# Optimization experiments

Measured on AMD Instinct MI355X. Metric: run time of the kernel, lower is better.

## Reference

```python
import math
import jax, jax.numpy as jnp
import numpy as np
from jax.scipy.special import erf

D = 128                # cubic box / image size (even)
B, T = 4, 2            # particles, candidate poses per particle
GRID_DIST_DEGS = 8.0
GRID_STEP_DEGS = 2.0
PIXEL_SIZE = 1.5       # Angstrom / px
MAX_SHIFT_FRACTION = 0.2
TOP_K = 2
HALF_PARTICLE = 0.5 * D


def _rot_z(a):
    c, s = jnp.cos(a), jnp.sin(a)
    z, o = jnp.zeros_like(a), jnp.ones_like(a)
    return jnp.stack([jnp.stack([c, -s, z], -1),
                      jnp.stack([s, c, z], -1),
                      jnp.stack([z, z, o], -1)], -2)


def _rot_y(a):
    c, s = jnp.cos(a), jnp.sin(a)
    z, o = jnp.zeros_like(a), jnp.ones_like(a)
    return jnp.stack([jnp.stack([c, z, s], -1),
                      jnp.stack([z, o, z], -1),
                      jnp.stack([-s, z, c], -1)], -2)


def _euler_zyz_to_matrix(ang):
    # RELION convention ZYZ: R = Rz(a) @ Ry(b) @ Rz(c)
    return _rot_z(ang[..., 0]) @ _rot_y(ang[..., 1]) @ _rot_z(ang[..., 2])


def _so3_grid_rotmats():
    n = math.ceil(GRID_DIST_DEGS / GRID_STEP_DEGS)
    n = n if n % 2 == 1 else n + 1
    half = GRID_DIST_DEGS / 2.0
    a = np.linspace(-half, half, n)
    g = np.stack(np.meshgrid(a, a, a, indexing='ij'), -1).reshape(-1, 3)
    return _euler_zyz_to_matrix(jnp.deg2rad(jnp.asarray(g, jnp.float32)))


def _compute_dft(vol):
    # sinc^2 gridding pre-filter, then fftshifted rfftn of fftshifted volume
    d = vol.shape[-1]
    f = jnp.fft.fftshift(jnp.fft.fftfreq(d)).astype(vol.dtype)
    fz, fy, fx = jnp.meshgrid(f, f, f, indexing='ij')
    r = jnp.sqrt(fz * fz + fy * fy + fx * fx)
    vol = vol * jnp.sinc(r) ** 2
    dft = jnp.fft.rfftn(jnp.fft.fftshift(vol, axes=(-3, -2, -1)), axes=(-3, -2, -1))
    return jnp.fft.fftshift(dft, axes=(-3, -2))


def _trilinear_complex(vol, z, y, x):
    # trilinear interpolation into a complex 3D array, zero outside bounds
    Dz, Dy, Dx = vol.shape
    z0f, y0f, x0f = jnp.floor(z), jnp.floor(y), jnp.floor(x)
    fz, fy, fx = z - z0f, y - y0f, x - x0f
    z0, y0, x0 = z0f.astype(jnp.int32), y0f.astype(jnp.int32), x0f.astype(jnp.int32)

    def corner(zi, yi, xi, w):
        valid = (zi >= 0) & (zi < Dz) & (yi >= 0) & (yi < Dy) & (xi >= 0) & (xi < Dx)
        v = vol[jnp.clip(zi, 0, Dz - 1), jnp.clip(yi, 0, Dy - 1), jnp.clip(xi, 0, Dx - 1)]
        return jnp.where(valid, v * w, jnp.zeros((), vol.dtype))

    out = corner(z0, y0, x0, (1 - fz) * (1 - fy) * (1 - fx))
    out = out + corner(z0, y0, x0 + 1, (1 - fz) * (1 - fy) * fx)
    out = out + corner(z0, y0 + 1, x0, (1 - fz) * fy * (1 - fx))
    out = out + corner(z0, y0 + 1, x0 + 1, (1 - fz) * fy * fx)
    out = out + corner(z0 + 1, y0, x0, fz * (1 - fy) * (1 - fx))
    out = out + corner(z0 + 1, y0, x0 + 1, fz * (1 - fy) * fx)
    out = out + corner(z0 + 1, y0 + 1, x0, fz * fy * (1 - fx))
    out = out + corner(z0 + 1, y0 + 1, x0 + 1, fz * fy * fx)
    return out


def _extract_central_slices_rfft_3d(vol_rfft, d, rotmats):
    # rotated central-slice extraction from a fftshifted rfft 3D volume
    fy = jnp.fft.fftshift(jnp.fft.fftfreq(d)).astype(jnp.float32)
    fx = jnp.fft.rfftfreq(d).astype(jnp.float32)
    gy, gx = jnp.meshgrid(fy, fx, indexing='ij')            # (H, Wr)
    coords = jnp.stack([jnp.zeros_like(gy), gy, gx], -1)    # zyx, z=0 plane
    Rzyx = rotmats[..., ::-1, ::-1]                         # xyz rotmat -> zyx
    rot = jnp.einsum('...ij,hwj->...hwi', Rzyx, coords)     # (...,H,Wr,3)
    conj_mask = rot[..., 2] < 0                             # redundant half
    rot = jnp.where(conj_mask[..., None], -rot, rot)
    zi = rot[..., 0] * d + d // 2
    yi = rot[..., 1] * d + d // 2
    xi = rot[..., 2] * d
    s = _trilinear_complex(vol_rfft, zi, yi, xi)
    return jnp.where(conj_mask, jnp.conj(s), s)


def _forward(vol, imgs, ctf, rotmats, grid_rotmats):
    d = vol.shape[-1]
    vol_rfft = _compute_dft(vol)                            # (d, d, d//2+1)
    # _real_to_fourier
    fimg = jnp.fft.fftshift(
        jnp.fft.rfftn(jnp.fft.fftshift(imgs, axes=(-2, -1)), axes=(-2, -1)),
        axes=(-2,))                                         # (B, d, d//2+1)
    # compose pose candidates with the local SO3 grid: rotmats @ grid_rotmats
    exp_R = jnp.einsum('gjk,btij->btgik', grid_rotmats, rotmats)   # (B,T,G,3,3)
    projs = _extract_central_slices_rfft_3d(vol_rfft, d, exp_R)    # (B,T,G,H,Wr)
    projs = projs * ctf[:, None, None]
    # correlate_dft_2d
    prod = fimg[:, None, None] * jnp.conj(projs)
    prod = jnp.fft.ifftshift(prod, axes=(-2,))
    corrs = jnp.fft.ifftshift(jnp.fft.irfftn(prod, s=(d, d), axes=(-2, -1)),
                              axes=(-2, -1))                # (B,T,G,d,d) real
    # constrained peak search within max_shift_fraction window
    delta = math.ceil(d * (1.0 - MAX_SHIFT_FRACTION) / 2)
    h0 = delta
    c = corrs[..., h0:d - delta, h0:d - delta]
    maxJ = jnp.max(c, -1)
    argJ = jnp.argmax(c, -1)
    perImgCorr = jnp.max(maxJ, -1)                          # (B,T,G)
    argI = jnp.argmax(maxJ, -1)
    col = jnp.take_along_axis(argJ, argI[..., None], -1)[..., 0]
    shiftsXY = jnp.stack([h0 + col, h0 + argI], -1)         # (B,T,G,2) as (x,y)
    b = perImgCorr.shape[0]
    nrots = perImgCorr.shape[2]
    flat = perImgCorr.reshape(b, -1)                        # (B, T*G)
    maxCorrs, maxIdxs = jax.lax.top_k(flat, TOP_K)
    bestShifts = jnp.take_along_axis(shiftsXY.reshape(b, -1, 2),
                                     maxIdxs[..., None], axis=1)   # (B,K,2)
    mean = jnp.mean(flat, -1, keepdims=True)
    std = jnp.std(flat, -1, keepdims=True, ddof=1)
    comparedWeight = 0.5 * (1.0 + erf((maxCorrs - mean) / (std * 1.4142135623730951)))
    predShiftsAngs = -(bestShifts.astype(jnp.float32) - HALF_PARTICLE) * PIXEL_SIZE
    predRotMats = grid_rotmats[maxIdxs % nrots]             # (B,K,3,3)
    return maxCorrs, predRotMats, predShiftsAngs, comparedWeight


def setup_inputs() -> dict:
    key = jax.random.key(0)
    kv, ki, kc, kr = jax.random.split(key, 4)
    vol = jax.random.normal(kv, (D, D, D), jnp.float32)
    imgs = jax.random.normal(ki, (B, D, D), jnp.float32)
    ctf = jax.random.uniform(kc, (B, D, D // 2 + 1), jnp.float32, -1.0, 1.0)
    ang = jax.random.uniform(kr, (B, T, 3), jnp.float32, -np.pi, np.pi)
    rotmats = _euler_zyz_to_matrix(ang)
    grid_rotmats = _so3_grid_rotmats()
    return {"vol": vol, "imgs": imgs, "ctf": ctf, "rotmats": rotmats,
            "grid_rotmats": grid_rotmats}


def reference(vol, imgs, ctf, rotmats, grid_rotmats):
    return _forward(vol, imgs, ctf, rotmats, grid_rotmats)
```

## Files before the change

### kernel.cpp

```cpp
#include <hip/hip_runtime.h>
#include <math.h>
#include <float.h>

#define DD   128
#define KX   65
#define NB   4
#define NTT  2
#define NG   125
#define NBTG (NB*NTT*NG)
#define WIN  24
#define H0   52

#define PZ  132
#define PY  132
#define PX  68
#define PROW  PX
#define PPLANE (PY*PX)
#define HALO_N 119872

typedef float f4 __attribute__((ext_vector_type(4), aligned(8)));

__device__ __forceinline__ float2 cmul(float2 a, float2 b){
    return make_float2(a.x*b.x - a.y*b.y, a.x*b.y + a.y*b.x);
}

__device__ __forceinline__ void make_tw(float2* sTw, int tid){
    if (tid < 128){
        float s, c;
        sincosf((float)tid * (float)(M_PI/64.0), &s, &c);
        sTw[tid] = make_float2(c, s);
    }
}

__global__ __launch_bounds__(256) void k_stageA(const float* __restrict__ vol,
                       const float* __restrict__ imgs,
                       float2* __restrict__ A1, float2* __restrict__ B1){
    __shared__ float2 sZ [16*DD];
    __shared__ float2 sZ2[16*DD];
    __shared__ float2 sTw[128];
    int tid = threadIdx.x;
    int bid = blockIdx.x;
    make_tw(sTw, tid);
    __syncthreads();

    if (bid < 512){
        int z = bid >> 2, q = bid & 3;
        int y0 = q*32;
        float fz = (z-64)*(1.0f/128.0f);
        for (int i = tid; i < 16*DD; i += 256){
            int p = i >> 7, x = i & 127;
            int yA = y0 + 2*p;
            float fx = (x-64)*(1.0f/128.0f);
            float fyA = (yA-64)*(1.0f/128.0f);
            float fyB = fyA + (1.0f/128.0f);
            float b2 = fz*fz + fx*fx;
            float rA = sqrtf(b2 + fyA*fyA);
            float rB = sqrtf(b2 + fyB*fyB);
            float sA = (rA > 0.f) ? (sinf((float)M_PI*rA)/((float)M_PI*rA)) : 1.f;
            float sB = (rB > 0.f) ? (sinf((float)M_PI*rB)/((float)M_PI*rB)) : 1.f;
            float a = vol[(z*DD + yA)*DD + x] * sA * sA;
            float b = vol[(z*DD + yA+1)*DD + x] * sB * sB;
            sZ[i] = make_float2(a, b);
        }
        __syncthreads();
        for (int i = tid; i < 16*32; i += 256){
            int p = i >> 5, x1 = i & 31;
            int b0 = p*DD + x1;
            float2 a = sZ[b0], bb = sZ[b0+32], c2 = sZ[b0+64], d = sZ[b0+96];
            float acx=a.x+c2.x, acy=a.y+c2.y;
            float amx=a.x-c2.x, amy=a.y-c2.y;
            float bdx=bb.x+d.x, bdy=bb.y+d.y;
            float bmx=bb.x-d.x, bmy=bb.y-d.y;
            sZ[b0   ] = make_float2(acx+bdx, acy+bdy);
            sZ[b0+32] = make_float2(amx+bmy, amy-bmx);
            sZ[b0+64] = make_float2(acx-bdx, acy-bdy);
            sZ[b0+96] = make_float2(amx-bmy, amy+bmx);
        }
        __syncthreads();
        for (int i = tid; i < 16*32; i += 256){
            int p = i >> 5, r5 = i & 31;
            int c = r5 >> 3, x2 = r5 & 7;
            int b0 = p*DD + 32*c + x2;
            float2 u0 = sZ[b0], u1 = sZ[b0+8], u2 = sZ[b0+16], u3 = sZ[b0+24];
            float2 w1 = sTw[(8*c)&127];  w1.y = -w1.y;
            float2 w2 = sTw[(16*c)&127]; w2.y = -w2.y;
            float2 w3 = sTw[(24*c)&127]; w3.y = -w3.y;
            float2 t1 = cmul(u1,w1), t2 = cmul(u2,w2), t3 = cmul(u3,w3);
            float2 pp = make_float2(u0.x+t2.x, u0.y+t2.y);
            float2 qq = make_float2(u0.x-t2.x, u0.y-t2.y);
            float2 rr = make_float2(t1.x+t3.x, t1.y+t3.y);
            float2 ss = make_float2(t1.x-t3.x, t1.y-t3.y);
            sZ[b0   ] = make_float2(pp.x+rr.x, pp.y+rr.y);
            sZ[b0+8 ] = make_float2(qq.x+ss.y, qq.y-ss.x);
            sZ[b0+16] = make_float2(pp.x-rr.x, pp.y-rr.y);
            sZ[b0+24] = make_float2(qq.x-ss.y, qq.y+ss.x);
        }
        __syncthreads();
        for (int i = tid; i < 16*DD; i += 256){
            int p = i >> 7, k = i & 127;
            int c = k & 3, s = (k >> 2) & 3;
            const float2* v = &sZ[p*DD + 32*c + 8*s];
            float ar0=0,ai0=0,ar1=0,ai1=0;
            int j = 0;
            #pragma unroll
            for (int x2 = 0; x2 < 8; x2 += 2){
                float2 v0 = v[x2], v1 = v[x2+1];
                float2 e0 = sTw[j]; int jn = (j + k)&127;
                float2 e1 = sTw[jn];
                ar0 += v0.x*e0.x + v0.y*e0.y;  ai0 += v0.y*e0.x - v0.x*e0.y;
                ar1 += v1.x*e1.x + v1.y*e1.y;  ai1 += v1.y*e1.x - v1.x*e1.y;
                j = (jn + k)&127;
            }
            sZ2[i] = make_float2(ar0+ar1, ai0+ai1);
        }
        __syncthreads();
        for (int i = tid; i < 16*KX; i += 256){
            int p = i / KX, k = i - p*KX;
            float2 Zk = sZ2[p*DD + k];
            float2 Zm = sZ2[p*DD + ((128-k)&127)];
            float2 A = make_float2(0.5f*(Zk.x+Zm.x), 0.5f*(Zk.y-Zm.y));
            float Dx = Zk.x - Zm.x, Dy = Zk.y + Zm.y;
            float2 Bv = make_float2(0.5f*Dy, -0.5f*Dx);
            int yA = y0 + 2*p;
            A1[(z*DD + yA  )*KX + k] = A;
            A1[(z*DD + yA+1)*KX + k] = Bv;
        }
    } else {
        int o = (bid - 512)*256 + tid;
        if (o >= NB*DD*KX) return;
        int b = o / (DD*KX);
        int r = o - b*DD*KX;
        int y = r / KX, k = r - y*KX;
        const float* row = imgs + (b*DD + y)*DD;
        float ar0=0,ai0=0,ar1=0,ai1=0,ar2=0,ai2=0,ar3=0,ai3=0;
        int i0=0, i1=k&127, i2=(2*k)&127, i3=(3*k)&127;
        int st = (4*k)&127;
        for (int x = 0; x < DD; x += 4){
            float v0=row[x], v1=row[x+1], v2=row[x+2], v3=row[x+3];
            float2 e0=sTw[i0], e1=sTw[i1], e2=sTw[i2], e3=sTw[i3];
            ar0 += v0*e0.x; ai0 -= v0*e0.y;
            ar1 += v1*e1.x; ai1 -= v1*e1.y;
            ar2 += v2*e2.x; ai2 -= v2*e2.y;
            ar3 += v3*e3.x; ai3 -= v3*e3.y;
            i0=(i0+st)&127; i1=(i1+st)&127; i2=(i2+st)&127; i3=(i3+st)&127;
        }
        B1[o] = make_float2(ar0+ar1+ar2+ar3, ai0+ai1+ai2+ai3);
    }
}

__global__ __launch_bounds__(256) void k_stageB(const float2* __restrict__ A1,
                       const float* __restrict__ ctf, const float2* __restrict__ B1,
                       float2* __restrict__ A2, float2* __restrict__ Fc){
    __shared__ float2 sU[32*KX];
    __shared__ float2 sTw[128];
    int tid = threadIdx.x;
    int bid = blockIdx.x;
    make_tw(sTw, tid);
    __syncthreads();

    if (bid < 512){
        int z = bid >> 2, c = bid & 3;
        const float2* base = A1 + z*DD*KX;
        for (int i = tid; i < 32*KX; i += 256){
            int n = i / KX, kk = i - n*KX;
            float2 a  = base[(n    )*KX + kk];
            float2 bb = base[(n+32)*KX + kk];
            float2 c2 = base[(n+64)*KX + kk];
            float2 d  = base[(n+96)*KX + kk];
            float acx = a.x + c2.x, acy = a.y + c2.y;
            float amx = a.x - c2.x, amy = a.y - c2.y;
            float bdx = bb.x + d.x, bdy = bb.y + d.y;
            float bmx = bb.x - d.x, bmy = bb.y - d.y;
            float2 u;
            if (c == 0)      u = make_float2(acx + bdx, acy + bdy);
            else if (c == 2) u = make_float2(acx - bdx, acy - bdy);
            else if (c == 1) u = make_float2(amx + bmy, amy - bmx);
            else             u = make_float2(amx - bmy, amy + bmx);
            sU[i] = u;
        }
        __syncthreads();
        float2 w1 = sTw[(8*c)&127];  w1.y = -w1.y;
        float2 w2 = sTw[(16*c)&127]; w2.y = -w2.y;
        float2 w3 = sTw[(24*c)&127]; w3.y = -w3.y;
        for (int i = tid; i < 8*KX; i += 256){
            int n2 = i / KX, kk = i - n2*KX;
            int b0 = n2*KX + kk;
            float2 u0 = sU[b0], u1 = sU[b0+8*KX], u2 = sU[b0+16*KX], u3 = sU[b0+24*KX];
            float2 t1 = cmul(u1,w1), t2 = cmul(u2,w2), t3 = cmul(u3,w3);
            float2 p = make_float2(u0.x+t2.x, u0.y+t2.y);
            float2 q = make_float2(u0.x-t2.x, u0.y-t2.y);
            float2 r = make_float2(t1.x+t3.x, t1.y+t3.y);
            float2 s = make_float2(t1.x-t3.x, t1.y-t3.y);
            sU[b0       ] = make_float2(p.x+r.x, p.y+r.y);
            sU[b0+ 8*KX ] = make_float2(q.x+s.y, q.y-s.x);
            sU[b0+16*KX ] = make_float2(p.x-r.x, p.y-r.y);
            sU[b0+24*KX ] = make_float2(q.x-s.y, q.y+s.x);
        }
        __syncthreads();
        for (int o = tid; o < 32*KX; o += 256){
            int m = o / KX, kk = o - m*KX;
            int ky = 4*m + c;
            int s4 = m & 3;
            const float2* v = &sU[(8*s4)*KX + kk];
            float ar0=0,ai0=0,ar1=0,ai1=0;
            int j = 0;
            #pragma unroll
            for (int n2 = 0; n2 < 8; n2 += 2){
                float2 v0 = v[n2*KX], v1 = v[(n2+1)*KX];
                float2 e0 = sTw[j]; int jn = (j + ky)&127;
                float2 e1 = sTw[jn];
                ar0 += v0.x*e0.x + v0.y*e0.y;  ai0 += v0.y*e0.x - v0.x*e0.y;
                ar1 += v1.x*e1.x + v1.y*e1.y;  ai1 += v1.y*e1.x - v1.x*e1.y;
                j = (jn + ky)&127;
            }
            A2[(z*DD + ky)*KX + kk] = make_float2(ar0+ar1, ai0+ai1);
        }
    } else {
        int o = (bid - 512)*256 + tid;
        if (o >= NB*DD*KX) return;
        int b = o / (DD*KX);
        int r = o - b*DD*KX;
        int h = r / KX, k = r - h*KX;
        int kky = (h + 64) & 127;
        const float2* col = B1 + b*DD*KX + k;
        float ar0=0,ai0=0,ar1=0,ai1=0,ar2=0,ai2=0,ar3=0,ai3=0;
        int i0=0, i1=kky&127, i2=(2*kky)&127, i3=(3*kky)&127;
        int st = (4*kky)&127;
        for (int y = 0; y < DD; y += 4){
            float2 v0=col[(y+0)*KX], v1=col[(y+1)*KX];
            float2 v2=col[(y+2)*KX], v3=col[(y+3)*KX];
            float2 e0=sTw[i0], e1=sTw[i1], e2=sTw[i2], e3=sTw[i3];
            ar0 += v0.x*e0.x + v0.y*e0.y;  ai0 += v0.y*e0.x - v0.x*e0.y;
            ar1 += v1.x*e1.x + v1.y*e1.y;  ai1 += v1.y*e1.x - v1.x*e1.y;
            ar2 += v2.x*e2.x + v2.y*e2.y;  ai2 += v2.y*e2.x - v2.x*e2.y;
            ar3 += v3.x*e3.x + v3.y*e3.y;  ai3 += v3.y*e3.x - v3.x*e3.y;
            i0=(i0+st)&127; i1=(i1+st)&127; i2=(i2+st)&127; i3=(i3+st)&127;
        }
        float sgn = ((h + k)&1) ? -1.f : 1.f;
        float cf = ctf[o];
        Fc[o] = make_float2((ar0+ar1+ar2+ar3)*sgn*cf, (ai0+ai1+ai2+ai3)*sgn*cf);
    }
}

__global__ __launch_bounds__(256) void k_volD(const float2* __restrict__ A2,
                       float2* __restrict__ VrP){
    __shared__ float2 sU[32*KX];
    __shared__ float2 sTw[128];
    int tid = threadIdx.x;
    int bid = blockIdx.x;
    int ky = bid >> 2, c = bid & 3;
    make_tw(sTw, tid);

    {
        int hidx = bid*256 + tid;
        if (hidx < HALO_N){
            int z, y, x;
            if (hidx < 35904){
                int p = hidx / 8976;
                int r = hidx - p*8976;
                z = (p == 0) ? 0 : (128 + p);
                y = r / 68;
                x = r - 68*y;
            } else if (hidx < 70720){
                int h2 = hidx - 35904;
                int zz = h2 / 272;
                int r = h2 - zz*272;
                z = 1 + zz;
                int p = r / 68;
                y = (p == 0) ? 0 : (128 + p);
                x = r - 68*p;
            } else {
                int h3 = hidx - 70720;
                int zz = h3 / 384;
                int r = h3 - zz*384;
                z = 1 + zz;
                y = 1 + r/3;
                x = 65 + (r - 3*(r/3));
            }
            VrP[(z*PY + y)*PX + x] = make_float2(0.f, 0.f);
        }
    }
    __syncthreads();

    const float2* base = A2 + ky*KX;
    for (int i = tid; i < 32*KX; i += 256){
        int n = i / KX, kk = i - n*KX;
        float2 a  = base[(n    )*DD*KX + kk];
        float2 bb = base[(n+32)*DD*KX + kk];
        float2 c2 = base[(n+64)*DD*KX + kk];
        float2 d  = base[(n+96)*DD*KX + kk];
        float acx = a.x + c2.x, acy = a.y + c2.y;
        float amx = a.x - c2.x, amy = a.y - c2.y;
        float bdx = bb.x + d.x, bdy = bb.y + d.y;
        float bmx = bb.x - d.x, bmy = bb.y - d.y;
        float2 u;
        if (c == 0)      u = make_float2(acx + bdx, acy + bdy);
        else if (c == 2) u = make_float2(acx - bdx, acy - bdy);
        else if (c == 1) u = make_float2(amx + bmy, amy - bmx);
        else             u = make_float2(amx - bmy, amy + bmx);
        sU[i] = u;
    }
    __syncthreads();
    float2 w1 = sTw[(8*c)&127];  w1.y = -w1.y;
    float2 w2 = sTw[(16*c)&127]; w2.y = -w2.y;
    float2 w3 = sTw[(24*c)&127]; w3.y = -w3.y;
    for (int i = tid; i < 8*KX; i += 256){
        int n2 = i / KX, kk = i - n2*KX;
        int b0 = n2*KX + kk;
        float2 u0 = sU[b0], u1 = sU[b0+8*KX], u2 = sU[b0+16*KX], u3 = sU[b0+24*KX];
        float2 t1 = cmul(u1,w1), t2 = cmul(u2,w2), t3 = cmul(u3,w3);
        float2 p = make_float2(u0.x+t2.x, u0.y+t2.y);
        float2 q = make_float2(u0.x-t2.x, u0.y-t2.y);
        float2 r = make_float2(t1.x+t3.x, t1.y+t3.y);
        float2 s = make_float2(t1.x-t3.x, t1.y-t3.y);
        sU[b0       ] = make_float2(p.x+r.x, p.y+r.y);
        sU[b0+ 8*KX ] = make_float2(q.x+s.y, q.y-s.x);
        sU[b0+16*KX ] = make_float2(p.x-r.x, p.y-r.y);
        sU[b0+24*KX ] = make_float2(q.x-s.y, q.y+s.x);
    }
    __syncthreads();
    int hy = (ky + 64) & 127;
    for (int o = tid; o < 32*KX; o += 256){
        int m = o / KX, kk = o - m*KX;
        int kz = 4*m + c;
        int hz = (kz + 64) & 127;
        int s4 = m & 3;
        const float2* v = &sU[(8*s4)*KX + kk];
        float ar0=0,ai0=0,ar1=0,ai1=0;
        int j = 0;
        #pragma unroll
        for (int n2 = 0; n2 < 8; n2 += 2){
            float2 v0 = v[n2*KX], v1 = v[(n2+1)*KX];
            float2 e0 = sTw[j]; int jn = (j + kz)&127;
            float2 e1 = sTw[jn];
            ar0 += v0.x*e0.x + v0.y*e0.y;  ai0 += v0.y*e0.x - v0.x*e0.y;
            ar1 += v1.x*e1.x + v1.y*e1.y;  ai1 += v1.y*e1.x - v1.x*e1.y;
            j = (jn + kz)&127;
        }
        float sgn = ((hz + hy + kk) & 1) ? -1.f : 1.f;
        VrP[((hz+1)*PY + (hy+1))*PX + kk] = make_float2((ar0+ar1)*sgn, (ai0+ai1)*sgn);
    }
}

__device__ __forceinline__ float2 slice_point(const float2* __restrict__ VrP,
        float2 f, float xi, float zi, float yi){
    bool neg = xi < 0.f;
    if (neg){ xi = -xi; zi = 128.f - zi; yi = 128.f - yi; }
    xi = fminf(xi, 65.f);
    zi = fminf(fmaxf(zi, -1.f), 129.f);
    yi = fminf(fmaxf(yi, -1.f), 129.f);
    float zf = floorf(zi), yf = floorf(yi), xf = floorf(xi);
    float fz = zi - zf, fy = yi - yf, fx = xi - xf;
    int z0 = (int)zf, y0 = (int)yf, x0 = (int)xf;
    int basei = ((z0+1)*PY + (y0+1))*PX + x0;
    f4 v00 = *reinterpret_cast<const f4*>(VrP + basei);
    f4 v01 = *reinterpret_cast<const f4*>(VrP + basei + PROW);
    f4 v10 = *reinterpret_cast<const f4*>(VrP + basei + PPLANE);
    f4 v11 = *reinterpret_cast<const f4*>(VrP + basei + PPLANE + PROW);
    float gx = 1.f - fx;
    float r00 = v00.x*gx + v00.z*fx, i00 = v00.y*gx + v00.w*fx;
    float r01 = v01.x*gx + v01.z*fx, i01 = v01.y*gx + v01.w*fx;
    float r10 = v10.x*gx + v10.z*fx, i10 = v10.y*gx + v10.w*fx;
    float r11 = v11.x*gx + v11.z*fx, i11 = v11.y*gx + v11.w*fx;
    float gz = 1.f - fz, gy = 1.f - fy;
    float w00 = gz*gy, w01 = gz*fy, w10 = fz*gy, w11 = fz*fy;
    float sr = r00*w00 + r01*w01 + r10*w10 + r11*w11;
    float si = i00*w00 + i01*w01 + i10*w10 + i11*w11;
    if (neg) si = -si;
    return make_float2(f.x*sr + f.y*si, f.y*sr - f.x*si);
}

__global__ __launch_bounds__(256,5) void k_main(
    const float2* __restrict__ VrP, const float2* __restrict__ Fc,
    const float* __restrict__ rotm, const float* __restrict__ grid,
    float* __restrict__ resVal, int2* __restrict__ resShift)
{
    __shared__ float2 sP[DD*16];
    __shared__ float2 sT[WIN*KX];
    __shared__ float2 sTw[128];
    __shared__ float  sM[9];
    __shared__ float  swv[4];
    __shared__ int    swi[4];

    int tid = threadIdx.x;
    int nb  = blockIdx.x;
    int blk = (nb & 7)*125 + (nb >> 3);
    int b  = blk / (NTT*NG);
    int rr = blk - b*NTT*NG;
    int t  = rr / NG;
    int g  = rr - t*NG;

    make_tw(sTw, tid);
    if (tid < 9){
        int i = tid/3, k = tid - 3*i;
        const float* R  = rotm + (b*NTT + t)*9;
        const float* Gm = grid + g*9;
        sM[tid] = R[i*3+0]*Gm[0*3+k] + R[i*3+1]*Gm[1*3+k] + R[i*3+2]*Gm[2*3+k];
    }
    __syncthreads();

    float M00=sM[0], M01=sM[1], M10=sM[3], M11=sM[4], M20=sM[6], M21=sM[7];
    const float2* FcB = Fc + b*DD*KX;

    if (tid < 128){
        int h = tid;
        float hf = (float)(h - 64);
        float xi = M01*hf + M00*64.f;
        float zi = M21*hf + M20*64.f + 64.f;
        float yi = M11*hf + M10*64.f + 64.f;
        sP[h] = slice_point(VrP, FcB[h*KX + 64], xi, zi, yi);
    }
    __syncthreads();
    if (tid < 96){
        int a = tid >> 2, p = tid & 3;
        int ry = (116 + a) & 127;
        int idx = (32*p*ry) & 127;
        float ar = 0.f, ai = 0.f;
        const float2* v = &sP[32*p];
        #pragma unroll 8
        for (int h2 = 0; h2 < 32; ++h2){
            float2 e = sTw[idx];
            float2 pv = v[h2];
            ar += pv.x*e.x - pv.y*e.y;
            ai += pv.x*e.y + pv.y*e.x;
            idx = (idx + ry) & 127;
        }
        sP[256 + tid] = make_float2(ar, ai);
    }
    __syncthreads();
    if (tid < 24){
        float2 p0 = sP[256 + tid*4 + 0];
        float2 p1 = sP[256 + tid*4 + 1];
        float2 p2 = sP[256 + tid*4 + 2];
        float2 p3 = sP[256 + tid*4 + 3];
        float sg = (tid & 1) ? -(1.f/128.f) : (1.f/128.f);
        sT[tid*KX + 64] = make_float2((p0.x+p1.x+p2.x+p3.x)*sg,
                                      (p0.y+p1.y+p2.y+p3.y)*sg);
    }
    __syncthreads();

    const int kk = tid & 15;
    const int h0 = tid >> 4;
    const float hf0 = (float)(h0 - 64);
    const float dxi = 16.f*M01, dzi = 16.f*M21, dyi = 16.f*M11;

    for (int cc = 0; cc < 4; ++cc){
        int w = cc*16 + kk;
        float wf = (float)w;
        float xi0 = M01*hf0 + M00*wf;
        float zi0 = M21*hf0 + M20*wf + 64.f;
        float yi0 = M11*hf0 + M10*wf + 64.f;
        int fidx = h0*KX + w;

        #pragma unroll 2
        for (int j = 0; j < 8; ++j){
            sP[tid + 256*j] = slice_point(VrP, FcB[fidx], xi0, zi0, yi0);
            xi0 += dxi; zi0 += dzi; yi0 += dyi; fidx += 16*KX;
        }
        __syncthreads();

        #pragma unroll
        for (int rep = 0; rep < 2; ++rep){
            int i = tid + 256*rep;
            float2 a  = sP[i];
            float2 bb = sP[i + 512];
            float2 c2 = sP[i + 1024];
            float2 d  = sP[i + 1536];
            float acx = a.x + c2.x, acy = a.y + c2.y;
            float amx = a.x - c2.x, amy = a.y - c2.y;
            float bdx = bb.x + d.x, bdy = bb.y + d.y;
            float bmx = bb.x - d.x, bmy = bb.y - d.y;
            sP[i       ] = make_float2(acx + bdx, acy + bdy);
            sP[i + 512 ] = make_float2(amx - bmy, amy + bmx);
            sP[i + 1024] = make_float2(acx - bdx, acy - bdy);
            sP[i + 1536] = make_float2(amx + bmy, amy - bmx);
        }
        __syncthreads();

        #pragma unroll
        for (int rep = 0; rep < 2; ++rep){
            int i = tid + 256*rep;
            int c = i >> 7, r7 = i & 127;
            int b0 = (c << 9) + r7;
            float2 u0 = sP[b0], u1 = sP[b0+128], u2 = sP[b0+256], u3 = sP[b0+384];
            float2 w1 = sTw[(8*c)&127], w2 = sTw[(16*c)&127], w3 = sTw[(24*c)&127];
            float2 t1 = cmul(u1,w1), t2 = cmul(u2,w2), t3 = cmul(u3,w3);
            float2 p  = make_float2(u0.x+t2.x, u0.y+t2.y);
            float2 qq = make_float2(u0.x-t2.x, u0.y-t2.y);
            float2 r  = make_float2(t1.x+t3.x, t1.y+t3.y);
            float2 s  = make_float2(t1.x-t3.x, t1.y-t3.y);
            sP[b0      ] = make_float2(p.x+r.x,  p.y+r.y);
            sP[b0 + 128] = make_float2(qq.x-s.y, qq.y+s.x);
            sP[b0 + 256] = make_float2(p.x-r.x,  p.y-r.y);
            sP[b0 + 384] = make_float2(qq.x+s.y, qq.y-s.x);
        }
        __syncthreads();

        for (int o = tid; o < 24*16; o += 256){
            int a = o >> 4, kx = o & 15;
            int ry = (116 + a) & 127;
            int c = ry & 3, s4 = (ry >> 2) & 3;
            const float2* v = &sP[(c << 9) + (s4 << 7) + kx];
            float ar0=0,ai0=0,ar1=0,ai1=0;
            int j2 = 0;
            #pragma unroll
            for (int n2 = 0; n2 < 8; n2 += 2){
                float2 v0 = v[n2*16], v1 = v[(n2+1)*16];
                float2 e0 = sTw[j2]; int jn = (j2 + ry)&127;
                float2 e1 = sTw[jn];
                ar0 += v0.x*e0.x - v0.y*e0.y;  ai0 += v0.x*e0.y + v0.y*e0.x;
                ar1 += v1.x*e1.x - v1.y*e1.y;  ai1 += v1.x*e1.y + v1.y*e1.x;
                j2 = (jn + ry)&127;
            }
            float sg = (a & 1) ? -(1.f/128.f) : (1.f/128.f);
            sT[a*KX + cc*16 + kx] = make_float2((ar0+ar1)*sg, (ai0+ai1)*sg);
        }
        __syncthreads();
    }

    float2* sPf = sP;
    for (int o = tid; o < WIN*31; o += 256){
        int a = o / 31, km1 = o - a*31;
        int k = km1 + 1;
        const float2* Trow = &sT[a*KX];
        float2 T1 = Trow[k], T2 = Trow[64-k];
        sPf[a*31 + km1]       = make_float2(T1.x + T2.x, T1.y - T2.y);
        sPf[744 + a*31 + km1] = make_float2(T1.x - T2.x, T1.y + T2.y);
    }
    __syncthreads();

    float* sC = reinterpret_cast<float*>(sP + 1488);
    for (int o = tid; o < WIN*WIN; o += 256){
        int a = o / WIN, bx = o - a*WIN;
        int rx = (116 + bx) & 127;
        const float2* Trow = &sT[a*KX];
        float2 T32 = Trow[32];
        float base = Trow[0].x + ((bx & 1) ? -Trow[64].x : Trow[64].x);
        int r4 = rx & 3;
        base += (r4==0) ?  2.f*T32.x : (r4==1) ? -2.f*T32.y
              : (r4==2) ? -2.f*T32.x :  2.f*T32.y;
        const float2* A = sPf + ((bx & 1) ? 744 : 0) + a*31 - 1;
        float acc0 = 0.f, acc1 = 0.f;
        int j1 = rx, j2 = (2*rx)&127;
        int st = (2*rx)&127;
        for (int k = 1; k < 31; k += 2){
            float2 e1 = sTw[j1]; float2 A1v = A[k];
            float2 e2 = sTw[j2]; float2 A2v = A[k+1];
            acc0 += A1v.x*e1.x - A1v.y*e1.y;
            acc1 += A2v.x*e2.x - A2v.y*e2.y;
            j1=(j1+st)&127; j2=(j2+st)&127;
        }
        {
            float2 e = sTw[(31*rx)&127]; float2 Av = A[31];
            acc0 += Av.x*e.x - Av.y*e.y;
        }
        sC[o] = (base + 2.f*(acc0+acc1))*(1.f/128.f);
    }
    __syncthreads();

    float best = -FLT_MAX; int bidx = 0x7fffffff;
    for (int i = tid; i < WIN*WIN; i += 256){
        float v = sC[i];
        if (v > best){ best = v; bidx = i; }
    }
    #pragma unroll
    for (int s = 32; s > 0; s >>= 1){
        float ov = __shfl_xor(best, s, 64);
        int   oi = __shfl_xor(bidx, s, 64);
        if (ov > best || (ov == best && oi < bidx)){ best = ov; bidx = oi; }
    }
    if ((tid & 63) == 0){ swv[tid>>6] = best; swi[tid>>6] = bidx; }
    __syncthreads();
    if (tid == 0){
        float bv = swv[0]; int bi = swi[0];
        #pragma unroll
        for (int w2 = 1; w2 < 4; ++w2){
            if (swv[w2] > bv || (swv[w2] == bv && swi[w2] < bi)){ bv = swv[w2]; bi = swi[w2]; }
        }
        int a = bi / WIN, bx = bi - a*WIN;
        resVal[blk] = bv;
        resShift[blk] = make_int2(H0 + bx, H0 + a);
    }
}

__global__ __launch_bounds__(256) void k_final(const float* __restrict__ resVal,
                        const int2* __restrict__ resShift,
                        const float* __restrict__ grid, float* __restrict__ out)
{
    __shared__ float sv[256];
    __shared__ int   si[256];
    __shared__ float sr[256];
    __shared__ float sMean;
    const int N = NTT*NG;
    int b = blockIdx.x, tid = threadIdx.x;
    const float* v = resVal + b*N;
    float myv = (tid < N) ? v[tid] : -FLT_MAX;

    sv[tid] = myv; si[tid] = (tid < N) ? tid : 0x7fffffff;
    __syncthreads();
    for (int s = 128; s > 0; s >>= 1){
        if (tid < s){
            float v2 = sv[tid+s]; int i2 = si[tid+s];
            if (v2 > sv[tid] || (v2 == sv[tid] && i2 < si[tid])){ sv[tid]=v2; si[tid]=i2; }
        }
        __syncthreads();
    }
    float v0 = sv[0]; int i0 = si[0];
    __syncthreads();

    bool act = (tid < N) && (tid != i0);
    sv[tid] = act ? myv : -FLT_MAX; si[tid] = act ? tid : 0x7fffffff;
    __syncthreads();
    for (int s = 128; s > 0; s >>= 1){
        if (tid < s){
            float v2 = sv[tid+s]; int i2 = si[tid+s];
            if (v2 > sv[tid] || (v2 == sv[tid] && i2 < si[tid])){ sv[tid]=v2; si[tid]=i2; }
        }
        __syncthreads();
    }
    float v1 = sv[0]; int i1 = si[0];
    __syncthreads();

    sr[tid] = (tid < N) ? myv : 0.f;
    __syncthreads();
    for (int s = 128; s > 0; s >>= 1){
        if (tid < s) sr[tid] += sr[tid+s];
        __syncthreads();
    }
    if (tid == 0) sMean = sr[0] / (float)N;
    __syncthreads();
    float mean = sMean;

    float d = (tid < N) ? (myv - mean) : 0.f;
    sr[tid] = d*d;
    __syncthreads();
    for (int s = 128; s > 0; s >>= 1){
        if (tid < s) sr[tid] += sr[tid+s];
        __syncthreads();
    }

    if (tid == 0){
        float stdv = sqrtf(sr[0] / (float)(N - 1));
        float vals[2] = {v0, v1};
        int   idxs[2] = {i0, i1};
        for (int k = 0; k < 2; ++k){
            out[b*2 + k] = vals[k];
            int gi = idxs[k] % NG;
            for (int j = 0; j < 9; ++j) out[8 + (b*2+k)*9 + j] = grid[gi*9 + j];
            int2 sh = resShift[b*N + idxs[k]];
            out[80 + (b*2+k)*2 + 0] = -((float)sh.x - 64.f)*1.5f;
            out[80 + (b*2+k)*2 + 1] = -((float)sh.y - 64.f)*1.5f;
            out[96 + b*2 + k] = 0.5f*(1.f + erff((vals[k] - mean)/(stdv*1.41421356237309515f)));
        }
    }
}

extern "C" void kernel_launch(void* const* d_in, const int* in_sizes, int n_in,
                              void* d_out, int out_size, void* d_ws, size_t ws_size,
                              hipStream_t stream)
{
    const float* vol  = (const float*)d_in[0];
    const float* imgs = (const float*)d_in[1];
    const float* ctf  = (const float*)d_in[2];
    const float* rotm = (const float*)d_in[3];
    const float* grid = (const float*)d_in[4];
    float* out = (float*)d_out;

    const size_t A1_BYTES  = (size_t)DD*DD*KX*sizeof(float2);
    const size_t B1_BYTES  = (size_t)NB*DD*KX*sizeof(float2);
    const size_t VRP_BYTES = (size_t)PZ*PY*PX*sizeof(float2);

    char* ws = (char*)d_ws;
    float2* A1  = (float2*)(ws);
    float2* B1  = (float2*)(ws + A1_BYTES);
    float2* VrP = (float2*)(ws);
    size_t off = VRP_BYTES;
    float2* A2 = (float2*)(ws + off); off += A1_BYTES;
    float2* Fc = (float2*)(ws + off); off += B1_BYTES;
    float* resVal = (float*)(ws + off); off += (size_t)NBTG*sizeof(float);
    int2* resShift = (int2*)(ws + off); off += (size_t)NBTG*sizeof(int2);

    k_stageA<<<642, 256, 0, stream>>>(vol, imgs, A1, B1);
    k_stageB<<<642, 256, 0, stream>>>(A1, ctf, B1, A2, Fc);
    k_volD  <<<512, 256, 0, stream>>>(A2, VrP);
    k_main  <<<NBTG,256, 0, stream>>>(VrP, Fc, rotm, grid, resVal, resShift);
    k_final <<<NB,  256, 0, stream>>>(resVal, resShift, grid, out);
}
```

Baseline: 117.5 us.

## Store padded volume with y-paired complex entries for 16-byte aligned gathers

The padded Fourier volume is rewritten so each entry holds the value at (z,y,x) together with its y+1 neighbour, making each trilinear sample four aligned 16-byte loads instead of four 8-byte-aligned loads of x pairs. The interpolation is reordered to blend x first, then y, then z on vector types. The volume doubles in size and must be fully zeroed by a new kernel launch, which replaces the halo-only zeroing inside k_volD. This adds memory traffic and one extra launch in exchange for aligned, wider gathers in the hot slice loop.

```diff
diff --git a/kernel.cpp b/kernel.cpp
--- a/kernel.cpp
+++ b/kernel.cpp
@@ -11,14 +11,14 @@
 #define WIN  24
 #define H0   52
 
-#define PZ  132
-#define PY  132
-#define PX  68
-#define PROW  PX
-#define PPLANE (PY*PX)
-#define HALO_N 119872
+#define QZ  132
+#define QY  131
+#define QX  68
+#define QPLANE (QY*QX)
+#define QN  (QZ*QY*QX)
 
 typedef float f4 __attribute__((ext_vector_type(4), aligned(8)));
+typedef float q4 __attribute__((ext_vector_type(4), aligned(16)));
 
 __device__ __forceinline__ float2 cmul(float2 a, float2 b){
     return make_float2(a.x*b.x - a.y*b.y, a.x*b.y + a.y*b.x);
@@ -242,44 +242,21 @@
     }
 }
 
+__global__ __launch_bounds__(256) void k_zero(float4* __restrict__ p){
+    int i = blockIdx.x*256 + threadIdx.x;
+    int n = QN;
+    for (; i < n; i += 256*2048)
+        p[i] = make_float4(0.f,0.f,0.f,0.f);
+}
+
 __global__ __launch_bounds__(256) void k_volD(const float2* __restrict__ A2,
-                       float2* __restrict__ VrP){
+                       float2* __restrict__ Yp2){
     __shared__ float2 sU[32*KX];
     __shared__ float2 sTw[128];
     int tid = threadIdx.x;
     int bid = blockIdx.x;
     int ky = bid >> 2, c = bid & 3;
     make_tw(sTw, tid);
-
-    {
-        int hidx = bid*256 + tid;
-        if (hidx < HALO_N){
-            int z, y, x;
-            if (hidx < 35904){
-                int p = hidx / 8976;
-                int r = hidx - p*8976;
-                z = (p == 0) ? 0 : (128 + p);
-                y = r / 68;
-                x = r - 68*y;
-            } else if (hidx < 70720){
-                int h2 = hidx - 35904;
-                int zz = h2 / 272;
-                int r = h2 - zz*272;
-                z = 1 + zz;
-                int p = r / 68;
-                y = (p == 0) ? 0 : (128 + p);
-                x = r - 68*p;
-            } else {
-                int h3 = hidx - 70720;
-                int zz = h3 / 384;
-                int r = h3 - zz*384;
-                z = 1 + zz;
-                y = 1 + r/3;
-                x = 65 + (r - 3*(r/3));
-            }
-            VrP[(z*PY + y)*PX + x] = make_float2(0.f, 0.f);
-        }
-    }
     __syncthreads();
 
     const float2* base = A2 + ky*KX;
@@ -338,11 +315,14 @@
             j = (jn + kz)&127;
         }
         float sgn = ((hz + hy + kk) & 1) ? -1.f : 1.f;
-        VrP[((hz+1)*PY + (hy+1))*PX + kk] = make_float2((ar0+ar1)*sgn, (ai0+ai1)*sgn);
-    }
-}
-
-__device__ __forceinline__ float2 slice_point(const float2* __restrict__ VrP,
+        float2 val = make_float2((ar0+ar1)*sgn, (ai0+ai1)*sgn);
+        int z = hz + 1, y = hy + 1;
+        Yp2[2*((z*QY + y    )*QX + kk)    ] = val;
+        Yp2[2*((z*QY + y - 1)*QX + kk) + 1] = val;
+    }
+}
+
+__device__ __forceinline__ float2 slice_point(const q4* __restrict__ Yp,
         float2 f, float xi, float zi, float yi){
     bool neg = xi < 0.f;
     if (neg){ xi = -xi; zi = 128.f - zi; yi = 128.f - yi; }
@@ -352,26 +332,22 @@
     float zf = floorf(zi), yf = floorf(yi), xf = floorf(xi);
     float fz = zi - zf, fy = yi - yf, fx = xi - xf;
     int z0 = (int)zf, y0 = (int)yf, x0 = (int)xf;
-    int basei = ((z0+1)*PY + (y0+1))*PX + x0;
-    f4 v00 = *reinterpret_cast<const f4*>(VrP + basei);
-    f4 v01 = *reinterpret_cast<const f4*>(VrP + basei + PROW);
-    f4 v10 = *reinterpret_cast<const f4*>(VrP + basei + PPLANE);
-    f4 v11 = *reinterpret_cast<const f4*>(VrP + basei + PPLANE + PROW);
+    int qi = ((z0+1)*QY + (y0+1))*QX + x0;
+    q4 a0 = Yp[qi],          a1 = Yp[qi + 1];
+    q4 b0 = Yp[qi + QPLANE], b1 = Yp[qi + QPLANE + 1];
     float gx = 1.f - fx;
-    float r00 = v00.x*gx + v00.z*fx, i00 = v00.y*gx + v00.w*fx;
-    float r01 = v01.x*gx + v01.z*fx, i01 = v01.y*gx + v01.w*fx;
-    float r10 = v10.x*gx + v10.z*fx, i10 = v10.y*gx + v10.w*fx;
-    float r11 = v11.x*gx + v11.z*fx, i11 = v11.y*gx + v11.w*fx;
-    float gz = 1.f - fz, gy = 1.f - fy;
-    float w00 = gz*gy, w01 = gz*fy, w10 = fz*gy, w11 = fz*fy;
-    float sr = r00*w00 + r01*w01 + r10*w10 + r11*w11;
-    float si = i00*w00 + i01*w01 + i10*w10 + i11*w11;
+    q4 A = a0*gx + a1*fx;
+    q4 B = b0*gx + b1*fx;
+    float gy = 1.f - fy, gz = 1.f - fz;
+    float cr = A.x*gy + A.z*fy, ci = A.y*gy + A.w*fy;
+    float dr = B.x*gy + B.z*fy, di = B.y*gy + B.w*fy;
+    float sr = cr*gz + dr*fz,   si = ci*gz + di*fz;
     if (neg) si = -si;
     return make_float2(f.x*sr + f.y*si, f.y*sr - f.x*si);
 }
 
 __global__ __launch_bounds__(256,5) void k_main(
-    const float2* __restrict__ VrP, const float2* __restrict__ Fc,
+    const q4* __restrict__ Yp, const float2* __restrict__ Fc,
     const float* __restrict__ rotm, const float* __restrict__ grid,
     float* __restrict__ resVal, int2* __restrict__ resShift)
 {
@@ -408,7 +384,7 @@
         float xi = M01*hf + M00*64.f;
         float zi = M21*hf + M20*64.f + 64.f;
         float yi = M11*hf + M10*64.f + 64.f;
-        sP[h] = slice_point(VrP, FcB[h*KX + 64], xi, zi, yi);
+        sP[h] = slice_point(Yp, FcB[h*KX + 64], xi, zi, yi);
     }
     __syncthreads();
     if (tid < 96){
@@ -454,7 +430,7 @@
 
         #pragma unroll 2
         for (int j = 0; j < 8; ++j){
-            sP[tid + 256*j] = slice_point(VrP, FcB[fidx], xi0, zi0, yi0);
+            sP[tid + 256*j] = slice_point(Yp, FcB[fidx], xi0, zi0, yi0);
             xi0 += dxi; zi0 += dzi; yi0 += dyi; fidx += 16*KX;
         }
         __syncthreads();
@@ -668,13 +644,13 @@
 
     const size_t A1_BYTES  = (size_t)DD*DD*KX*sizeof(float2);
     const size_t B1_BYTES  = (size_t)NB*DD*KX*sizeof(float2);
-    const size_t VRP_BYTES = (size_t)PZ*PY*PX*sizeof(float2);
+    const size_t YP_BYTES  = (size_t)QN*16;
 
     char* ws = (char*)d_ws;
-    float2* A1  = (float2*)(ws);
-    float2* B1  = (float2*)(ws + A1_BYTES);
-    float2* VrP = (float2*)(ws);
-    size_t off = VRP_BYTES;
+    float2* A1 = (float2*)(ws);
+    float2* B1 = (float2*)(ws + A1_BYTES);
+    q4*     Yp = (q4*)(ws);
+    size_t off = YP_BYTES;
     float2* A2 = (float2*)(ws + off); off += A1_BYTES;
     float2* Fc = (float2*)(ws + off); off += B1_BYTES;
     float* resVal = (float*)(ws + off); off += (size_t)NBTG*sizeof(float);
@@ -682,7 +658,8 @@
 
     k_stageA<<<642, 256, 0, stream>>>(vol, imgs, A1, B1);
     k_stageB<<<642, 256, 0, stream>>>(A1, ctf, B1, A2, Fc);
-    k_volD  <<<512, 256, 0, stream>>>(A2, VrP);
-    k_main  <<<NBTG,256, 0, stream>>>(VrP, Fc, rotm, grid, resVal, resShift);
+    k_zero  <<<2048,256, 0, stream>>>((float4*)Yp);
+    k_volD  <<<512, 256, 0, stream>>>(A2, (float2*)Yp);
+    k_main  <<<NBTG,256, 0, stream>>>(Yp, Fc, rotm, grid, resVal, resShift);
     k_final <<<NB,  256, 0, stream>>>(resVal, resShift, grid, out);
 }
```

Result: slower. 141.7 us (+20.6%).
